# Performance work log

Measured on AMD Instinct MI355X. Metric: run time of the kernel, lower is better.

## Reference

```python
import jax, jax.numpy as jnp
import numpy as np


def setup_inputs() -> dict:
    key = jax.random.key(0)
    k = jax.random.split(key, 5)
    B, S, D, H = 4, 2048, 2048, 8192
    scale1 = 1.0 / np.sqrt(D)
    scale2 = 1.0 / np.sqrt(H)
    return {
        "x": jax.random.normal(k[0], (B, S, D), dtype=jnp.float32),
        "w1": jax.random.normal(k[1], (H, D), dtype=jnp.float32) * scale1,
        "b1": jax.random.normal(k[2], (H,), dtype=jnp.float32) * scale1,
        "w2": jax.random.normal(k[3], (D, H), dtype=jnp.float32) * scale2,
        "b2": jax.random.normal(k[4], (D,), dtype=jnp.float32) * scale2,
    }


def reference(x, w1, b1, w2, b2):
    # fc1: [B,S,D] @ [D,H] -> [B,S,H]
    h = jnp.einsum("bsd,hd->bsh", x, w1) + b1
    # squared ReLU activation
    a = jnp.square(jax.nn.relu(h))
    # fc2: [B,S,H] @ [H,D] -> [B,S,D]
    return jnp.einsum("bsh,dh->bsd", a, w2) + b2
```

## Files before the change

kernel.cpp:

```cpp
#include <hip/hip_runtime.h>
#include <hip/hip_bf16.h>
#include <stdint.h>

typedef __bf16 bf16x8 __attribute__((ext_vector_type(8)));
typedef float f32x4 __attribute__((ext_vector_type(4)));


__device__ inline void gload_lds16(const void* g, void* lds) {
  __builtin_amdgcn_global_load_lds(
      (const __attribute__((address_space(1))) uint32_t*)(uintptr_t)g,
      (__attribute__((address_space(3))) uint32_t*)(uintptr_t)lds,
      16, 0, 0);
}

__device__ inline short f2bf(float f) {
  union { float f; uint32_t u; } x; x.f = f;
  uint32_t u = x.u;
  u += 0x7fffu + ((u >> 16) & 1u);
  return (short)(u >> 16);
}

#define BAR() do { asm volatile("" ::: "memory"); \
                   __builtin_amdgcn_s_barrier();  \
                   asm volatile("" ::: "memory"); } while (0)


__global__ __launch_bounds__(256) void cvt_f32_bf16(
    const float* __restrict__ in, short* __restrict__ out, int n4) {
  int i = blockIdx.x * 256 + threadIdx.x;
  if (i < n4) {
    float4 v = reinterpret_cast<const float4*>(in)[i];
    short4 o;
    o.x = f2bf(v.x); o.y = f2bf(v.y); o.z = f2bf(v.z); o.w = f2bf(v.w);
    reinterpret_cast<short4*>(out)[i] = o;
  }
}


template <int EPI>
__global__ __launch_bounds__(512, 2) void gemm_bt(
    const short* __restrict__ A, const short* __restrict__ B,
    const float* __restrict__ bias, void* __restrict__ Cout,
    int M, int N, int K) {
  __shared__ __align__(16) short lds[2][4][128 * 64];

  const int tid  = threadIdx.x;
  const int wave = tid >> 6;
  const int lane = tid & 63;
  const int wr = wave >> 2;
  const int wc = wave & 3;
  const int fr = lane & 15, kq = lane >> 4;

  const int nwg = gridDim.x;
  const int w = (blockIdx.x & 7) * (nwg >> 3) + (blockIdx.x >> 3);
  const int gy = M >> 8;
  const int brow = w % gy;
  const int bcol = w / gy;

  f32x4 acc[8][4];
#pragma unroll
  for (int m = 0; m < 8; ++m)
#pragma unroll
    for (int n = 0; n < 4; ++n)
      acc[m][n] = (f32x4){0.f, 0.f, 0.f, 0.f};

  const int nk = K >> 6;

  int offA[4][2], offB[2][2];
#pragma unroll
  for (int m = 0; m < 4; ++m)
#pragma unroll
    for (int kk = 0; kk < 2; ++kk) {
      int r = wr * 64 + m * 16 + fr;
      int g = r * 8 + kk * 4 + kq;
      offA[m][kk] = (g ^ (r & 7)) * 16;
    }
#pragma unroll
  for (int n = 0; n < 2; ++n)
#pragma unroll
    for (int kk = 0; kk < 2; ++kk) {
      int r = wc * 32 + n * 16 + fr;
      int g = r * 8 + kk * 4 + kq;
      offB[n][kk] = (g ^ (r & 7)) * 16;
    }

  const int i0 = tid;
  const int gl0 = i0 ^ ((i0 >> 3) & 7);
  const int r0 = gl0 >> 3, c0 = gl0 & 7;
  const size_t rstep = (size_t)128 * K;

  const short* pA[2];
  const short* pB[2];
  {
    const int rb0 = (r0 >> 5) * 64 + (r0 & 31);
#pragma unroll
    for (int h = 0; h < 2; ++h) {
      pA[h] = A + (size_t)(brow * 256 + h * 64 + r0) * K + c0 * 8;
      pB[h] = B + (size_t)(bcol * 256 + rb0 + h * 32) * K + c0 * 8;
    }
  }

  const int dst0 = wave * 512, dst1 = 4096 + wave * 512;

#define STAGE(p, buf, slot)                              \
  do {                                                   \
    short* base_ = &lds[buf][slot][0];                   \
    gload_lds16((p), base_ + dst0);                      \
    gload_lds16((p) + rstep, base_ + dst1);              \
    (p) += 64;                                           \
  } while (0)

  STAGE(pA[0], 0, 0);
  STAGE(pB[0], 0, 2);
  STAGE(pB[1], 0, 3);
  STAGE(pA[1], 0, 1);
  STAGE(pA[0], 1, 0);
  STAGE(pB[0], 1, 2);
  STAGE(pB[1], 1, 3);
  asm volatile("s_waitcnt vmcnt(6)" ::: "memory");
  BAR();

  bf16x8 aq[4][2], b0q[2][2], b1q[2][2];

  for (int t = 0; t < nk; ++t) {
    const int cur = t & 1, nxt = cur ^ 1;
    const bool s1 = (t + 1) < nk, s2 = (t + 2) < nk;

    if (s1) STAGE(pA[1], nxt, 1);
    {
      const char* sA = (const char*)&lds[cur][0][0];
      const char* sB = (const char*)&lds[cur][2][0];
#pragma unroll
      for (int m = 0; m < 4; ++m)
#pragma unroll
        for (int kk = 0; kk < 2; ++kk)
          aq[m][kk] = *(const bf16x8*)(sA + offA[m][kk]);
#pragma unroll
      for (int n = 0; n < 2; ++n)
#pragma unroll
        for (int kk = 0; kk < 2; ++kk)
          b0q[n][kk] = *(const bf16x8*)(sB + offB[n][kk]);
    }
    BAR();
    __builtin_amdgcn_s_setprio(1);
#pragma unroll
    for (int m = 0; m < 4; ++m)
#pragma unroll
      for (int n = 0; n < 2; ++n)
#pragma unroll
        for (int kk = 0; kk < 2; ++kk)
          acc[m][n] = __builtin_amdgcn_mfma_f32_16x16x32_bf16(
              aq[m][kk], b0q[n][kk], acc[m][n], 0, 0, 0);
    __builtin_amdgcn_s_setprio(0);
    BAR();

    if (s2) STAGE(pA[0], cur, 0);
    {
      const char* sB = (const char*)&lds[cur][3][0];
#pragma unroll
      for (int n = 0; n < 2; ++n)
#pragma unroll
        for (int kk = 0; kk < 2; ++kk)
          b1q[n][kk] = *(const bf16x8*)(sB + offB[n][kk]);
    }
    BAR();
    __builtin_amdgcn_s_setprio(1);
#pragma unroll
    for (int m = 0; m < 4; ++m)
#pragma unroll
      for (int n = 0; n < 2; ++n)
#pragma unroll
        for (int kk = 0; kk < 2; ++kk)
          acc[m][n + 2] = __builtin_amdgcn_mfma_f32_16x16x32_bf16(
              aq[m][kk], b1q[n][kk], acc[m][n + 2], 0, 0, 0);
    __builtin_amdgcn_s_setprio(0);
    BAR();

    if (s2) STAGE(pB[0], cur, 2);
    {
      const char* sA = (const char*)&lds[cur][1][0];
#pragma unroll
      for (int m = 0; m < 4; ++m)
#pragma unroll
        for (int kk = 0; kk < 2; ++kk)
          aq[m][kk] = *(const bf16x8*)(sA + offA[m][kk]);
    }
    BAR();
    __builtin_amdgcn_s_setprio(1);
#pragma unroll
    for (int m = 0; m < 4; ++m)
#pragma unroll
      for (int n = 0; n < 2; ++n)
#pragma unroll
        for (int kk = 0; kk < 2; ++kk)
          acc[m + 4][n + 2] = __builtin_amdgcn_mfma_f32_16x16x32_bf16(
              aq[m][kk], b1q[n][kk], acc[m + 4][n + 2], 0, 0, 0);
    __builtin_amdgcn_s_setprio(0);
    BAR();

    if (s2) STAGE(pB[1], cur, 3);
    BAR();
    __builtin_amdgcn_s_setprio(1);
#pragma unroll
    for (int m = 0; m < 4; ++m)
#pragma unroll
      for (int n = 0; n < 2; ++n)
#pragma unroll
        for (int kk = 0; kk < 2; ++kk)
          acc[m + 4][n] = __builtin_amdgcn_mfma_f32_16x16x32_bf16(
              aq[m][kk], b0q[n][kk], acc[m + 4][n], 0, 0, 0);
    __builtin_amdgcn_s_setprio(0);

    if (t < nk - 1) {
      if (s2) asm volatile("s_waitcnt vmcnt(6)" ::: "memory");
      else    asm volatile("s_waitcnt vmcnt(0)" ::: "memory");
      BAR();
    }
  }

  const int q = lane >> 4;
  if (EPI == 0) {
    short* C = (short*)Cout;
#pragma unroll
    for (int m = 0; m < 8; ++m) {
      const int row0 = brow * 256 + wr * 128 + m * 16 + q * 4;
#pragma unroll
      for (int n = 0; n < 4; ++n) {
        const int col = bcol * 256 + wc * 64 + n * 16 + fr;
        const float bv = bias[col];
#pragma unroll
        for (int j = 0; j < 4; ++j) {
          float v = acc[m][n][j] + bv;
          v = v > 0.f ? v * v : 0.f;
          C[(size_t)(row0 + j) * N + col] = f2bf(v);
        }
      }
    }
  } else {
    float* C = (float*)Cout;
#pragma unroll
    for (int m = 0; m < 8; ++m) {
      const int row0 = brow * 256 + wr * 128 + m * 16 + q * 4;
#pragma unroll
      for (int n = 0; n < 4; ++n) {
        const int col = bcol * 256 + wc * 64 + n * 16 + fr;
        const float bv = bias[col];
#pragma unroll
        for (int j = 0; j < 4; ++j)
          C[(size_t)(row0 + j) * N + col] = acc[m][n][j] + bv;
      }
    }
  }
#undef STAGE
}


extern "C" void kernel_launch(void* const* d_in, const int* in_sizes, int n_in,
                              void* d_out, int out_size, void* d_ws,
                              size_t ws_size, hipStream_t stream) {
  const float* x  = (const float*)d_in[0];
  const float* w1 = (const float*)d_in[1];
  const float* b1 = (const float*)d_in[2];
  const float* w2 = (const float*)d_in[3];
  const float* b2 = (const float*)d_in[4];
  float* out = (float*)d_out;

  const int H = in_sizes[2];
  const int D = in_sizes[4];
  const int M = in_sizes[0] / D;

  short* xb  = (short*)d_ws;
  short* w1b = xb  + (size_t)M * D;
  short* w2b = w1b + (size_t)H * D;
  short* act = w2b + (size_t)D * H;

  {
    int n4 = (M * D) / 4;
    cvt_f32_bf16<<<(n4 + 255) / 256, 256, 0, stream>>>(x, xb, n4);
    n4 = (H * D) / 4;
    cvt_f32_bf16<<<(n4 + 255) / 256, 256, 0, stream>>>(w1, w1b, n4);
    n4 = (D * H) / 4;
    cvt_f32_bf16<<<(n4 + 255) / 256, 256, 0, stream>>>(w2, w2b, n4);
  }

  gemm_bt<0><<<(M / 256) * (H / 256), 512, 0, stream>>>(
      xb, w1b, b1, (void*)act, M, H, D);
  gemm_bt<1><<<(M / 256) * (D / 256), 512, 0, stream>>>(
      act, w2b, b2, (void*)out, M, D, H);
}
```

Before: 548.8 us.

## Simplify GEMM main loop to whole-tile double buffering with one barrier

Replaces the interleaved four-phase schedule with a plain double buffer. The old schedule issued partial-tile loads between MFMA groups, used several barriers per iteration and waited with vmcnt(6). Now all four next-tile loads are issued at the top of each iteration, both A halves and both B halves are read from LDS into separate registers, all MFMAs run, and then a full vmcnt(0) wait and a single barrier follow. This cuts barrier count, but it keeps more operand registers live under a tight launch bound and gives a coarser overlap between memory and MFMA work.

Measured after the change: 559.4 us. No clear change (+1.9%).

```diff
diff --git a/kernel.cpp b/kernel.cpp
--- a/kernel.cpp
+++ b/kernel.cpp
@@ -111,37 +111,47 @@
   } while (0)
 
   STAGE(pA[0], 0, 0);
+  STAGE(pA[1], 0, 1);
   STAGE(pB[0], 0, 2);
   STAGE(pB[1], 0, 3);
-  STAGE(pA[1], 0, 1);
-  STAGE(pA[0], 1, 0);
-  STAGE(pB[0], 1, 2);
-  STAGE(pB[1], 1, 3);
-  asm volatile("s_waitcnt vmcnt(6)" ::: "memory");
+  asm volatile("s_waitcnt vmcnt(0)" ::: "memory");
   BAR();
 
-  bf16x8 aq[4][2], b0q[2][2], b1q[2][2];
+  bf16x8 a0q[4][2], a1q[4][2], bq0[2][2], bq1[2][2];
 
   for (int t = 0; t < nk; ++t) {
     const int cur = t & 1, nxt = cur ^ 1;
-    const bool s1 = (t + 1) < nk, s2 = (t + 2) < nk;
-
-    if (s1) STAGE(pA[1], nxt, 1);
-    {
-      const char* sA = (const char*)&lds[cur][0][0];
-      const char* sB = (const char*)&lds[cur][2][0];
-#pragma unroll
-      for (int m = 0; m < 4; ++m)
-#pragma unroll
-        for (int kk = 0; kk < 2; ++kk)
-          aq[m][kk] = *(const bf16x8*)(sA + offA[m][kk]);
-#pragma unroll
-      for (int n = 0; n < 2; ++n)
-#pragma unroll
-        for (int kk = 0; kk < 2; ++kk)
-          b0q[n][kk] = *(const bf16x8*)(sB + offB[n][kk]);
-    }
-    BAR();
+    const bool s1 = (t + 1) < nk;
+
+    if (s1) {
+      STAGE(pA[0], nxt, 0);
+      STAGE(pA[1], nxt, 1);
+      STAGE(pB[0], nxt, 2);
+      STAGE(pB[1], nxt, 3);
+    }
+
+    const char* sA0 = (const char*)&lds[cur][0][0];
+    const char* sA1 = (const char*)&lds[cur][1][0];
+    const char* sB0 = (const char*)&lds[cur][2][0];
+    const char* sB1 = (const char*)&lds[cur][3][0];
+
+#pragma unroll
+    for (int m = 0; m < 4; ++m)
+#pragma unroll
+      for (int kk = 0; kk < 2; ++kk)
+        a0q[m][kk] = *(const bf16x8*)(sA0 + offA[m][kk]);
+#pragma unroll
+    for (int n = 0; n < 2; ++n)
+#pragma unroll
+      for (int kk = 0; kk < 2; ++kk)
+        bq0[n][kk] = *(const bf16x8*)(sB0 + offB[n][kk]);
+
+#pragma unroll
+    for (int m = 0; m < 4; ++m)
+#pragma unroll
+      for (int kk = 0; kk < 2; ++kk)
+        a1q[m][kk] = *(const bf16x8*)(sA1 + offA[m][kk]);
+
     __builtin_amdgcn_s_setprio(1);
 #pragma unroll
     for (int m = 0; m < 4; ++m)
@@ -150,20 +160,26 @@
 #pragma unroll
         for (int kk = 0; kk < 2; ++kk)
           acc[m][n] = __builtin_amdgcn_mfma_f32_16x16x32_bf16(
-              aq[m][kk], b0q[n][kk], acc[m][n], 0, 0, 0);
-    __builtin_amdgcn_s_setprio(0);
-    BAR();
-
-    if (s2) STAGE(pA[0], cur, 0);
-    {
-      const char* sB = (const char*)&lds[cur][3][0];
-#pragma unroll
-      for (int n = 0; n < 2; ++n)
-#pragma unroll
-        for (int kk = 0; kk < 2; ++kk)
-          b1q[n][kk] = *(const bf16x8*)(sB + offB[n][kk]);
-    }
-    BAR();
+              a0q[m][kk], bq0[n][kk], acc[m][n], 0, 0, 0);
+    __builtin_amdgcn_s_setprio(0);
+
+#pragma unroll
+    for (int n = 0; n < 2; ++n)
+#pragma unroll
+      for (int kk = 0; kk < 2; ++kk)
+        bq1[n][kk] = *(const bf16x8*)(sB1 + offB[n][kk]);
+
+    __builtin_amdgcn_s_setprio(1);
+#pragma unroll
+    for (int m = 0; m < 4; ++m)
+#pragma unroll
+      for (int n = 0; n < 2; ++n)
+#pragma unroll
+        for (int kk = 0; kk < 2; ++kk)
+          acc[m + 4][n] = __builtin_amdgcn_mfma_f32_16x16x32_bf16(
+              a1q[m][kk], bq0[n][kk], acc[m + 4][n], 0, 0, 0);
+    __builtin_amdgcn_s_setprio(0);
+
     __builtin_amdgcn_s_setprio(1);
 #pragma unroll
     for (int m = 0; m < 4; ++m)
@@ -172,20 +188,9 @@
 #pragma unroll
         for (int kk = 0; kk < 2; ++kk)
           acc[m][n + 2] = __builtin_amdgcn_mfma_f32_16x16x32_bf16(
-              aq[m][kk], b1q[n][kk], acc[m][n + 2], 0, 0, 0);
-    __builtin_amdgcn_s_setprio(0);
-    BAR();
-
-    if (s2) STAGE(pB[0], cur, 2);
-    {
-      const char* sA = (const char*)&lds[cur][1][0];
-#pragma unroll
-      for (int m = 0; m < 4; ++m)
-#pragma unroll
-        for (int kk = 0; kk < 2; ++kk)
-          aq[m][kk] = *(const bf16x8*)(sA + offA[m][kk]);
-    }
-    BAR();
+              a0q[m][kk], bq1[n][kk], acc[m][n + 2], 0, 0, 0);
+    __builtin_amdgcn_s_setprio(0);
+
     __builtin_amdgcn_s_setprio(1);
 #pragma unroll
     for (int m = 0; m < 4; ++m)
@@ -194,26 +199,11 @@
 #pragma unroll
         for (int kk = 0; kk < 2; ++kk)
           acc[m + 4][n + 2] = __builtin_amdgcn_mfma_f32_16x16x32_bf16(
-              aq[m][kk], b1q[n][kk], acc[m + 4][n + 2], 0, 0, 0);
-    __builtin_amdgcn_s_setprio(0);
-    BAR();
-
-    if (s2) STAGE(pB[1], cur, 3);
-    BAR();
-    __builtin_amdgcn_s_setprio(1);
-#pragma unroll
-    for (int m = 0; m < 4; ++m)
-#pragma unroll
-      for (int n = 0; n < 2; ++n)
-#pragma unroll
-        for (int kk = 0; kk < 2; ++kk)
-          acc[m + 4][n] = __builtin_amdgcn_mfma_f32_16x16x32_bf16(
-              aq[m][kk], b0q[n][kk], acc[m + 4][n], 0, 0, 0);
-    __builtin_amdgcn_s_setprio(0);
-
-    if (t < nk - 1) {
-      if (s2) asm volatile("s_waitcnt vmcnt(6)" ::: "memory");
-      else    asm volatile("s_waitcnt vmcnt(0)" ::: "memory");
+              a1q[m][kk], bq1[n][kk], acc[m + 4][n + 2], 0, 0, 0);
+    __builtin_amdgcn_s_setprio(0);
+
+    if (s1) {
+      asm volatile("s_waitcnt vmcnt(0)" ::: "memory");
       BAR();
     }
   }
```
